# Performance work log

Hardware: AMD Instinct MI355X
Metric: run time of the kernel (lower is better)

The kernel has to match this reference:

```python
import jax, jax.numpy as jnp
import numpy as np

B, NCROPS, T = 512, 5, 8192
NEG = -1e30  # masked fill for invalid (beyond-seqlen) positions


def setup_inputs() -> dict:
    key = jax.random.key(0)
    k1, k2, k3 = jax.random.split(key, 3)
    scores = jax.random.normal(k1, (B * NCROPS, T), dtype=jnp.float32)
    label = jax.random.randint(k2, (B,), 0, 2, dtype=jnp.int32)
    # valid lengths in [16, T] so that k = seqlen//16 + 1 is always in range
    seqlen = jax.random.randint(k3, (B,), 16, T + 1, dtype=jnp.int32)
    return {"scores": scores, "label": label, "seqlen": seqlen}


def reference(scores, label, seqlen):
    # uncrop 'mean': [B*ncrops, T] -> [B, T]
    s = scores.reshape(B, NCROPS, T).mean(axis=1)

    # mask invalid positions, sort each row descending (vectorized ragged top-k)
    valid = jnp.arange(T)[None, :] < seqlen[:, None]            # [B, T]
    s_sorted = -jnp.sort(-jnp.where(valid, s, NEG), axis=1)     # descending
    csum = jnp.cumsum(s_sorted, axis=1)                         # [B, T]

    # get_k: label==0 -> 1; k==-1 -> seqlen//16 + 1 (k-1 < seqlen always)
    k = jnp.where(label == 0, 1, seqlen // 16 + 1)              # [B]
    topk_sum = jnp.take_along_axis(csum, (k - 1)[:, None], axis=1)[:, 0]
    vl_scores = topk_sum / k.astype(s.dtype)                    # mean of top-k

    # BCEWithLogitsLoss (mean reduction): logaddexp(0, v) - v*y
    y = label.astype(s.dtype)
    loss = jnp.mean(jnp.logaddexp(0.0, vl_scores) - vl_scores * y)
    return loss
```

## Files before the change

### kernel.cpp

```cpp
#include <hip/hip_runtime.h>
#include <stdint.h>

#define BB      512
#define NCROPS  5
#define TT      8192
#define THREADS 512
#define WAVES   8
#define HPAD    257

__device__ __forceinline__ uint32_t f2ord(float f) {
    uint32_t b = __float_as_uint(f);
    return (b & 0x80000000u) ? ~b : (b | 0x80000000u);
}
__device__ __forceinline__ float ord2f(uint32_t u) {
    uint32_t b = (u & 0x80000000u) ? (u & 0x7FFFFFFFu) : ~u;
    return __uint_as_float(b);
}

#define FOR4(OP) OP(u0) OP(u1) OP(u2) OP(u3)

__global__ __launch_bounds__(THREADS, 2) void topk_loss_rows(
    const float* __restrict__ scores, const int* __restrict__ label,
    const int* __restrict__ seqlen, float* __restrict__ row_loss)
{
    const int b    = blockIdx.x;
    const int tid  = threadIdx.x;
    const int lane = tid & 63;
    const int wave = tid >> 6;

    const int sl = seqlen[b];
    const int lb = label[b];
    const int k  = (lb == 0) ? 1 : (sl / 16 + 1);

    __shared__ uint32_t hist[2][WAVES][HPAD];
    __shared__ uint32_t bc_p, bc_k;
    __shared__ uint32_t s_m[WAVES];
    __shared__ float    s_s[WAVES];
    __shared__ int      s_c[WAVES];
    __shared__ uint32_t s_pad[17000];
    if (sl == -2147483647) s_pad[tid] = 0u;

    const float* base = scores + (size_t)b * NCROPS * TT;
    #define LOADJ(A0,A1,A2,A3,A4, J, PRED) \
        const bool PRED = (4 * (tid + (J) * THREADS) < sl); \
        float4 A0, A1, A2, A3, A4; \
        if (PRED) { \
            const int t4 = tid + (J) * THREADS; \
            A0 = *reinterpret_cast<const float4*>(base + 0 * TT + 4 * t4); \
            A1 = *reinterpret_cast<const float4*>(base + 1 * TT + 4 * t4); \
            A2 = *reinterpret_cast<const float4*>(base + 2 * TT + 4 * t4); \
            A3 = *reinterpret_cast<const float4*>(base + 3 * TT + 4 * t4); \
            A4 = *reinterpret_cast<const float4*>(base + 4 * TT + 4 * t4); \
        }
    LOADJ(a0,b0,c0,d0,e0, 0, p0)
    LOADJ(a1,b1,c1,d1,e1, 1, p1)
    LOADJ(a2,b2,c2,d2,e2, 2, p2)
    LOADJ(a3,b3,c3,d3,e3, 3, p3)

    {
        uint32_t* hz = &hist[0][0][0];
        for (int i = tid; i < WAVES * HPAD; i += THREADS) hz[i] = 0u;
    }
    __syncthreads();

    uint4 u0, u1, u2, u3;
    #define KEYJ(DST, A0,A1,A2,A3,A4, J, PRED) \
        if (PRED) { \
            const int t0 = 4 * (tid + (J) * THREADS); \
            float4 a; \
            a.x = (A0.x + A1.x + A2.x + A3.x + A4.x) * 0.2f; \
            a.y = (A0.y + A1.y + A2.y + A3.y + A4.y) * 0.2f; \
            a.z = (A0.z + A1.z + A2.z + A3.z + A4.z) * 0.2f; \
            a.w = (A0.w + A1.w + A2.w + A3.w + A4.w) * 0.2f; \
            DST.x = f2ord(a.x); \
            DST.y = (t0 + 1 < sl) ? f2ord(a.y) : 0u; \
            DST.z = (t0 + 2 < sl) ? f2ord(a.z) : 0u; \
            DST.w = (t0 + 3 < sl) ? f2ord(a.w) : 0u; \
        } else { \
            DST.x = 0u; DST.y = 0u; DST.z = 0u; DST.w = 0u; \
        }
    KEYJ(u0, a0,b0,c0,d0,e0, 0, p0)
    KEYJ(u1, a1,b1,c1,d1,e1, 1, p1)
    KEYJ(u2, a2,b2,c2,d2,e2, 2, p2)
    KEYJ(u3, a3,b3,c3,d3,e3, 3, p3)

    uint32_t thr;
    if (k == 1) {
        uint32_t mx = 0u;
        #define MAXOP(V) mx = max(mx, max(max(V.x, V.y), max(V.z, V.w)));
        FOR4(MAXOP)
        #pragma unroll
        for (int off = 32; off; off >>= 1) {
            const uint32_t o = (uint32_t)__shfl_down((int)mx, off);
            mx = max(mx, o);
        }
        if (lane == 0) s_m[wave] = mx;
        __syncthreads();
        uint32_t rowmax = s_m[0];
        #pragma unroll
        for (int w = 1; w < WAVES; ++w) rowmax = max(rowmax, s_m[w]);
        thr = rowmax;
    } else {
        uint32_t p = 0u, kr = (uint32_t)k;
        #pragma unroll
        for (int r = 0; r < 4; ++r) {
            uint32_t* h = &hist[r & 1][wave][0];
            if (r == 0) {
                #define H0(X)  if ((X) != 0u) atomicAdd(&h[(X) >> 24], 1u);
                #define H0V(V) H0(V.x) H0(V.y) H0(V.z) H0(V.w)
                FOR4(H0V)
            } else {
                const int shp = 32 - 8 * r;
                const int shd = shp - 8;
                #define HR(X)  if ((X) != 0u && ((X) >> shp) == p) atomicAdd(&h[((X) >> shd) & 255u], 1u);
                #define HRV(V) HR(V.x) HR(V.y) HR(V.z) HR(V.w)
                FOR4(HRV)
            }
            __syncthreads();
            if (wave == 0) {
                uint32_t t0s = 0u, t1s = 0u, t2s = 0u, t3s = 0u;
                #pragma unroll
                for (int w = 0; w < WAVES; ++w) {
                    const uint32_t* hw = &hist[r & 1][w][0];
                    t0s += hw[4 * lane + 0];
                    t1s += hw[4 * lane + 1];
                    t2s += hw[4 * lane + 2];
                    t3s += hw[4 * lane + 3];
                }
                const uint32_t s = t0s + t1s + t2s + t3s;
                uint32_t suf = s;
                #pragma unroll
                for (int off = 1; off < 64; off <<= 1) {
                    const uint32_t v = (uint32_t)__shfl_down((int)suf, off);
                    if (lane + off < 64) suf += v;
                }
                const uint32_t E  = suf - s;
                const uint32_t T3 = E  + t3s;
                const uint32_t T2 = T3 + t2s;
                const uint32_t T1 = T2 + t1s;
                const uint32_t T0 = T1 + t0s;
                const unsigned long long bal = __ballot(T0 >= kr);
                const int L = 63 - __clzll(bal);
                if (lane == L) {
                    uint32_t j, Tj, tj;
                    if      (T3 >= kr) { j = 3u; Tj = T3; tj = t3s; }
                    else if (T2 >= kr) { j = 2u; Tj = T2; tj = t2s; }
                    else if (T1 >= kr) { j = 1u; Tj = T1; tj = t1s; }
                    else               { j = 0u; Tj = T0; tj = t0s; }
                    bc_p = (p << 8) | (uint32_t)(4 * lane) | j;
                    bc_k = kr - (Tj - tj);
                }
            } else if (r < 3) {
                uint32_t* hz = &hist[(r + 1) & 1][0][0];
                for (int i = tid - 64; i < WAVES * HPAD; i += (THREADS - 64)) hz[i] = 0u;
            }
            __syncthreads();
            p  = bc_p;
            kr = bc_k;
        }
        thr = p;
    }

    float sg = 0.f;
    int   cg = 0;
    #define SUMOP(V) \
        if (V.x >= thr) { sg += ord2f(V.x); cg++; } \
        if (V.y >= thr) { sg += ord2f(V.y); cg++; } \
        if (V.z >= thr) { sg += ord2f(V.z); cg++; } \
        if (V.w >= thr) { sg += ord2f(V.w); cg++; }
    FOR4(SUMOP)
    #pragma unroll
    for (int off = 32; off; off >>= 1) {
        sg += __shfl_down(sg, off);
        cg += __shfl_down(cg, off);
    }
    if (lane == 0) { s_s[wave] = sg; s_c[wave] = cg; }
    __syncthreads();

    if (tid == 0) {
        float S = 0.f; int C = 0;
        #pragma unroll
        for (int w = 0; w < WAVES; ++w) { S += s_s[w]; C += s_c[w]; }
        const float kf   = ord2f(thr);
        const float topk = S - (float)(C - k) * kf;
        const float v    = topk / (float)k;
        const float y    = (float)lb;
        const float la   = fmaxf(v, 0.f) + log1pf(expf(-fabsf(v)));
        row_loss[b] = la - v * y;
    }
}

__global__ __launch_bounds__(256) void reduce_loss(
    const float* __restrict__ row_loss, float* __restrict__ out)
{
    const int tid = threadIdx.x;
    float v = row_loss[tid] + row_loss[tid + 256];
    #pragma unroll
    for (int off = 32; off; off >>= 1) v += __shfl_down(v, off);
    __shared__ float s[4];
    if ((tid & 63) == 0) s[tid >> 6] = v;
    __syncthreads();
    if (tid == 0) out[0] = (s[0] + s[1] + s[2] + s[3]) * (1.0f / 512.0f);
}

extern "C" void kernel_launch(void* const* d_in, const int* in_sizes, int n_in,
                              void* d_out, int out_size, void* d_ws, size_t ws_size,
                              hipStream_t stream) {
    const float* scores = (const float*)d_in[0];
    const int*   label  = (const int*)d_in[1];
    const int*   seqlen = (const int*)d_in[2];
    float* out      = (float*)d_out;
    float* row_loss = (float*)d_ws;

    topk_loss_rows<<<BB, THREADS, 0, stream>>>(scores, label, seqlen, row_loss);
    reduce_loss<<<1, 256, 0, stream>>>(row_loss, out);
}
```

Baseline: 22.61 us.

## Split crop-mean into separate wide kernel writing ordered keys to workspace

Moves the 5-crop mean and float-to-ordered-key conversion into a new kernel launched with 8 blocks per row, which writes keys to a workspace buffer. The selection kernel then reads only the keys, drops the large shared-memory padding array, and raises its occupancy hint from 2 to 4 blocks. The aim is more memory-level parallelism for the dominant streaming read. The cost is an extra global round trip for the keys (write then read about 16 MB at most) and one more kernel launch.

```diff
diff --git a/kernel.cpp b/kernel.cpp
--- a/kernel.cpp
+++ b/kernel.cpp
@@ -17,10 +17,43 @@
     return __uint_as_float(b);
 }
 
+__global__ __launch_bounds__(256) void mean_keys(
+    const float* __restrict__ scores, const int* __restrict__ seqlen,
+    uint32_t* __restrict__ keys)
+{
+    const int bid = blockIdx.x;
+    const int r   = bid >> 3;
+    const int c   = bid & 7;
+    const int sl  = seqlen[r];
+    if (c * 1024 >= sl) return;
+
+    const int t4 = c * 256 + threadIdx.x;
+    const int t0 = 4 * t4;
+    if (t0 >= sl) return;
+
+    const float* base = scores + (size_t)r * NCROPS * TT;
+    float4 a        = *reinterpret_cast<const float4*>(base + 0 * TT + t0);
+    const float4 v1 = *reinterpret_cast<const float4*>(base + 1 * TT + t0);
+    const float4 v2 = *reinterpret_cast<const float4*>(base + 2 * TT + t0);
+    const float4 v3 = *reinterpret_cast<const float4*>(base + 3 * TT + t0);
+    const float4 v4 = *reinterpret_cast<const float4*>(base + 4 * TT + t0);
+    a.x = (a.x + v1.x + v2.x + v3.x + v4.x) * 0.2f;
+    a.y = (a.y + v1.y + v2.y + v3.y + v4.y) * 0.2f;
+    a.z = (a.z + v1.z + v2.z + v3.z + v4.z) * 0.2f;
+    a.w = (a.w + v1.w + v2.w + v3.w + v4.w) * 0.2f;
+
+    uint4 kv;
+    kv.x = f2ord(a.x);
+    kv.y = (t0 + 1 < sl) ? f2ord(a.y) : 0u;
+    kv.z = (t0 + 2 < sl) ? f2ord(a.z) : 0u;
+    kv.w = (t0 + 3 < sl) ? f2ord(a.w) : 0u;
+    *reinterpret_cast<uint4*>(keys + (size_t)r * TT + t0) = kv;
+}
+
 #define FOR4(OP) OP(u0) OP(u1) OP(u2) OP(u3)
 
-__global__ __launch_bounds__(THREADS, 2) void topk_loss_rows(
-    const float* __restrict__ scores, const int* __restrict__ label,
+__global__ __launch_bounds__(THREADS, 4) void select_loss(
+    const uint32_t* __restrict__ keys, const int* __restrict__ label,
     const int* __restrict__ seqlen, float* __restrict__ row_loss)
 {
     const int b    = blockIdx.x;
@@ -37,52 +70,23 @@
     __shared__ uint32_t s_m[WAVES];
     __shared__ float    s_s[WAVES];
     __shared__ int      s_c[WAVES];
-    __shared__ uint32_t s_pad[17000];
-    if (sl == -2147483647) s_pad[tid] = 0u;
-
-    const float* base = scores + (size_t)b * NCROPS * TT;
-    #define LOADJ(A0,A1,A2,A3,A4, J, PRED) \
-        const bool PRED = (4 * (tid + (J) * THREADS) < sl); \
-        float4 A0, A1, A2, A3, A4; \
-        if (PRED) { \
-            const int t4 = tid + (J) * THREADS; \
-            A0 = *reinterpret_cast<const float4*>(base + 0 * TT + 4 * t4); \
-            A1 = *reinterpret_cast<const float4*>(base + 1 * TT + 4 * t4); \
-            A2 = *reinterpret_cast<const float4*>(base + 2 * TT + 4 * t4); \
-            A3 = *reinterpret_cast<const float4*>(base + 3 * TT + 4 * t4); \
-            A4 = *reinterpret_cast<const float4*>(base + 4 * TT + 4 * t4); \
-        }
-    LOADJ(a0,b0,c0,d0,e0, 0, p0)
-    LOADJ(a1,b1,c1,d1,e1, 1, p1)
-    LOADJ(a2,b2,c2,d2,e2, 2, p2)
-    LOADJ(a3,b3,c3,d3,e3, 3, p3)
+
+    const uint32_t* kbase = keys + (size_t)b * TT;
+    uint4 u0, u1, u2, u3;
+    #define KLOADJ(DST, J) { \
+        const int t4 = tid + (J) * THREADS; \
+        if (4 * t4 < sl) DST = *reinterpret_cast<const uint4*>(kbase + 4 * t4); \
+        else { DST.x = 0u; DST.y = 0u; DST.z = 0u; DST.w = 0u; } }
+    KLOADJ(u0, 0)
+    KLOADJ(u1, 1)
+    KLOADJ(u2, 2)
+    KLOADJ(u3, 3)
 
     {
         uint32_t* hz = &hist[0][0][0];
         for (int i = tid; i < WAVES * HPAD; i += THREADS) hz[i] = 0u;
     }
     __syncthreads();
-
-    uint4 u0, u1, u2, u3;
-    #define KEYJ(DST, A0,A1,A2,A3,A4, J, PRED) \
-        if (PRED) { \
-            const int t0 = 4 * (tid + (J) * THREADS); \
-            float4 a; \
-            a.x = (A0.x + A1.x + A2.x + A3.x + A4.x) * 0.2f; \
-            a.y = (A0.y + A1.y + A2.y + A3.y + A4.y) * 0.2f; \
-            a.z = (A0.z + A1.z + A2.z + A3.z + A4.z) * 0.2f; \
-            a.w = (A0.w + A1.w + A2.w + A3.w + A4.w) * 0.2f; \
-            DST.x = f2ord(a.x); \
-            DST.y = (t0 + 1 < sl) ? f2ord(a.y) : 0u; \
-            DST.z = (t0 + 2 < sl) ? f2ord(a.z) : 0u; \
-            DST.w = (t0 + 3 < sl) ? f2ord(a.w) : 0u; \
-        } else { \
-            DST.x = 0u; DST.y = 0u; DST.z = 0u; DST.w = 0u; \
-        }
-    KEYJ(u0, a0,b0,c0,d0,e0, 0, p0)
-    KEYJ(u1, a1,b1,c1,d1,e1, 1, p1)
-    KEYJ(u2, a2,b2,c2,d2,e2, 2, p2)
-    KEYJ(u3, a3,b3,c3,d3,e3, 3, p3)
 
     uint32_t thr;
     if (k == 1) {
@@ -209,9 +213,13 @@
     const float* scores = (const float*)d_in[0];
     const int*   label  = (const int*)d_in[1];
     const int*   seqlen = (const int*)d_in[2];
-    float* out      = (float*)d_out;
-    float* row_loss = (float*)d_ws;
-
-    topk_loss_rows<<<BB, THREADS, 0, stream>>>(scores, label, seqlen, row_loss);
+    float* out = (float*)d_out;
+
+    const size_t keys_bytes = (size_t)BB * TT * sizeof(uint32_t);
+    uint32_t* keys     = (uint32_t*)d_ws;
+    float*    row_loss = (float*)((char*)d_ws + keys_bytes);
+
+    mean_keys<<<BB * 8, 256, 0, stream>>>(scores, seqlen, keys);
+    select_loss<<<BB, THREADS, 0, stream>>>(keys, label, seqlen, row_loss);
     reduce_loss<<<1, 256, 0, stream>>>(row_loss, out);
 }
```

After: 33.13 us. +46.5%, slower.
